# Optimization experiments

Measured on AMD Instinct MI355X. Metric: run time of the kernel, lower is better.

The kernel has to match this reference:

```python
import jax, jax.numpy as jnp
import numpy as np
import math

B, T, D, H = 4, 1024, 1024, 16
DK = D // H
TAU_THRESH = 0.3


def setup_inputs() -> dict:
    key = jax.random.key(0)
    ks = jax.random.split(key, 13)
    s = 1.0 / math.sqrt(D)
    return {
        "x": jax.random.normal(ks[0], (B, T, D), dtype=jnp.float32),
        "Wq": jax.random.normal(ks[1], (D, D), dtype=jnp.float32) * s,
        "bq": jax.random.normal(ks[2], (D,), dtype=jnp.float32) * s,
        "Wk": jax.random.normal(ks[3], (D, D), dtype=jnp.float32) * s,
        "bk": jax.random.normal(ks[4], (D,), dtype=jnp.float32) * s,
        "Wv": jax.random.normal(ks[5], (D, D), dtype=jnp.float32) * s,
        "bv": jax.random.normal(ks[6], (D,), dtype=jnp.float32) * s,
        "Wo": jax.random.normal(ks[7], (D, D), dtype=jnp.float32) * s,
        "bo": jax.random.normal(ks[8], (D,), dtype=jnp.float32) * s,
        "Wg1": jax.random.normal(ks[9], (1, D), dtype=jnp.float32) * s,
        "bg1": jax.random.normal(ks[10], (1,), dtype=jnp.float32) * s,
        "Wg2": jax.random.normal(ks[11], (1, D), dtype=jnp.float32) * s,
        "bg2": jax.random.normal(ks[12], (1,), dtype=jnp.float32) * s,
    }


def reference(x, Wq, bq, Wk, bk, Wv, bv, Wo, bo, Wg1, bg1, Wg2, bg2):
    b, t, d = x.shape
    # projections (torch Linear: y = x @ W.T + b)
    Q = (x @ Wq.T + bq).reshape(b, t, H, DK).transpose(0, 2, 1, 3)  # [B,H,T,dk]
    K = (x @ Wk.T + bk).reshape(b, t, H, DK).transpose(0, 2, 1, 3)
    V = (x @ Wv.T + bv).reshape(b, t, H, DK).transpose(0, 2, 1, 3)
    scores = jnp.einsum("bhqd,bhkd->bhqk", Q, K) / math.sqrt(DK)  # [B,H,T,T]
    # confidence gates from first-token query context [B, H*dk] = [B, D]
    context = Q[:, :, 0, :].reshape(b, d)
    q1 = jax.nn.sigmoid(context @ Wg1.T + bg1)  # [B,1]
    q2 = jax.nn.sigmoid(context @ Wg2.T + bg2)  # [B,1]
    c = jnp.clip(q1 * q2, 1e-8, 1.0)            # [B,1]
    tau = jnp.where(c < TAU_THRESH, 1.0 / c, jnp.ones_like(c)).reshape(b, 1, 1, 1)
    p = jax.nn.softmax(scores / tau, axis=-1)
    cb = c.reshape(b, 1, 1, 1)
    p_gated = cb * p + (1.0 - cb) * (1.0 / t)
    u = jnp.mean(1.0 - c, axis=-1, keepdims=True)  # [B,1]
    attn_out = jnp.einsum("bhqk,bhkd->bhqd", p_gated, V)
    attn_out = attn_out.transpose(0, 2, 1, 3).reshape(b, t, d)
    output = attn_out @ Wo.T + bo
    return output, u
```

## Files before the change

kernel.cpp:

```cpp
#include <hip/hip_runtime.h>
#include <stdint.h>

typedef short bf16x8 __attribute__((ext_vector_type(8)));
typedef float f32x4 __attribute__((ext_vector_type(4)));

#define MFMA_BF16(a, b, c) __builtin_amdgcn_mfma_f32_16x16x32_bf16((a), (b), (c), 0, 0, 0)

__device__ __forceinline__ short f2bf(float x) {
  union { float f; uint32_t u; } v; v.f = x;
  uint32_t r = (v.u + 0x7FFFu + ((v.u >> 16) & 1u)) >> 16;
  return (short)r;
}
__device__ __forceinline__ uint32_t rnd_bf_hi(float x) {
  union { float f; uint32_t u; } v; v.f = x;
  return v.u + 0x7FFFu + ((v.u >> 16) & 1u);
}
__device__ __forceinline__ uint32_t pack2bf(float a, float b) {
  return __builtin_amdgcn_perm(rnd_bf_hi(b), rnd_bf_hi(a), 0x07060302);
}
__device__ __forceinline__ float bfbits2f(uint32_t b16) {
  union { uint32_t u; float f; } v; v.u = b16 << 16; return v.f;
}
__device__ __forceinline__ float fexp2(float x) {
#if __has_builtin(__builtin_amdgcn_exp2f)
  return __builtin_amdgcn_exp2f(x);
#else
  return __expf(x * 0.6931471805599453f);
#endif
}
__device__ __forceinline__ void async16(const void* g, void* l) {
  __builtin_amdgcn_global_load_lds(
      (const __attribute__((address_space(1))) uint32_t*)g,
      (__attribute__((address_space(3))) uint32_t*)l, 16, 0, 0);
}

#define BAR() __builtin_amdgcn_s_barrier()
#define LGKM0() asm volatile("s_waitcnt lgkmcnt(0)" ::: "memory")
#define VMCNT(n) asm volatile("s_waitcnt vmcnt(" #n ")" ::: "memory")
#define PRIO1() __builtin_amdgcn_s_setprio(1)
#define PRIO0() __builtin_amdgcn_s_setprio(0)

__global__ __launch_bounds__(256) void prep_k(
    const float* __restrict__ x, const float* __restrict__ Wq,
    const float* __restrict__ Wk, const float* __restrict__ Wv,
    const float* __restrict__ Wo, const float* __restrict__ bq,
    short* __restrict__ xb, short* __restrict__ Wqb, short* __restrict__ Wkb,
    short* __restrict__ Wvb, short* __restrict__ Wob, float* __restrict__ ctx) {
  __shared__ float xs[1024];
  const int bid = blockIdx.x;
  const int tid = threadIdx.x;
  if (bid < 8192) {
    const float* src; short* dst; int idx;
    if (bid < 4096) {
      src = x; dst = xb; idx = (bid << 8) + tid;
    } else {
      const int r = bid - 4096;
      const int z = r >> 10;
      src = (z == 0) ? Wq : (z == 1) ? Wk : (z == 2) ? Wv : Wo;
      dst = (z == 0) ? Wqb : (z == 1) ? Wkb : (z == 2) ? Wvb : Wob;
      idx = ((r & 1023) << 8) + tid;
    }
    float4 v = ((const float4*)src)[idx];
    short4 o;
    o.x = f2bf(v.x); o.y = f2bf(v.y); o.z = f2bf(v.z); o.w = f2bf(v.w);
    ((short4*)dst)[idx] = o;
  } else {
    const int r = bid - 8192;
    const int b = r >> 4;
    const int n0 = (r & 15) << 6;
    for (int i = tid; i < 1024; i += 256) xs[i] = x[b * 1048576 + i];
    __syncthreads();
    const int w = tid >> 6, lane = tid & 63;
    const float4* xv4 = (const float4*)xs;
    for (int rr = 0; rr < 16; ++rr) {
      const int n = n0 + (w << 4) + rr;
      const float4* wrow = (const float4*)(Wq + n * 1024);
      float p = 0.f;
#pragma unroll
      for (int c2 = 0; c2 < 4; ++c2) {
        float4 wv = wrow[lane + (c2 << 6)];
        float4 xv = xv4[lane + (c2 << 6)];
        p += xv.x * wv.x + xv.y * wv.y + xv.z * wv.z + xv.w * wv.w;
      }
#pragma unroll
      for (int off = 32; off; off >>= 1) p += __shfl_xor(p, off);
      if (lane == 0) ctx[b * 1024 + n] = p + bq[n];
    }
  }
}

__global__ __launch_bounds__(256) void gates_fin(const float* __restrict__ ctx,
                                                 const float* __restrict__ Wg1,
                                                 const float* __restrict__ bg1,
                                                 const float* __restrict__ Wg2,
                                                 const float* __restrict__ bg2,
                                                 float* __restrict__ gates,
                                                 float* __restrict__ u_out) {
  __shared__ float red[16];
  const int tid = threadIdx.x, w = tid >> 6, lane = tid & 63;
  for (int b = 0; b < 4; ++b) {
    float4 cv = ((const float4*)(ctx + b * 1024))[tid];
    float4 w1 = ((const float4*)Wg1)[tid];
    float4 w2 = ((const float4*)Wg2)[tid];
    float p1 = cv.x * w1.x + cv.y * w1.y + cv.z * w1.z + cv.w * w1.w;
    float p2 = cv.x * w2.x + cv.y * w2.y + cv.z * w2.z + cv.w * w2.w;
#pragma unroll
    for (int off = 32; off; off >>= 1) { p1 += __shfl_xor(p1, off); p2 += __shfl_xor(p2, off); }
    if (lane == 0) { red[w] = p1; red[8 + w] = p2; }
    __syncthreads();
    if (tid == 0) {
      float g1 = red[0] + red[1] + red[2] + red[3] + bg1[0];
      float g2 = red[8] + red[9] + red[10] + red[11] + bg2[0];
      float q1 = 1.f / (1.f + expf(-g1));
      float q2 = 1.f / (1.f + expf(-g2));
      float c = fminf(fmaxf(q1 * q2, 1e-8f), 1.0f);
      gates[b * 2 + 0] = c;
      gates[b * 2 + 1] = (c < 0.3f ? c : 1.0f) * 0.125f * 1.4426950408889634f;
      u_out[b] = 1.0f - c;
    }
    __syncthreads();
  }
}

template <bool SWP>
__device__ __forceinline__ void qkv_core(const short* __restrict__ xb,
                                         const short* __restrict__ W,
                                         const float* __restrict__ bias,
                                         short* __restrict__ out,
                                         short* sm, int m0, int nl0) {
  const int tid = threadIdx.x;
  const int wid = tid >> 6, lane = tid & 63;
  const int wr = wid >> 2, wc = wid & 3;
  const int m15 = lane & 15, quad = lane >> 4;

  const int rowb = tid >> 3;
  const int c16 = (tid & 7) ^ (((tid >> 5) & 1) << 1);
  const short* aB = xb + (m0 + rowb) * 1024 + (c16 << 3);
  const short* bB = W + (nl0 + rowb) * 1024 + (c16 << 3);

  short* As = sm;
  short* Bs = sm + 32768;

#define STAGEH(sb, tt, hf, dst)                        \
  do {                                                 \
    const short* _s = (sb) + (hf)*131072 + (tt)*64;    \
    short* _d = (dst) + ((hf) << 13) + (tid << 3);     \
    async16(_s, _d);                                   \
    async16(_s + 65536, _d + 4096);                    \
  } while (0)

#define RD(base, f, kk)                                                        \
  (*(const bf16x8*)((base) + ((f) << 10) + (m15 << 6) +                        \
                    (((((kk) << 2) + quad) ^ ((m15 & 4) >> 1)) << 3)))

#define MM(accr, af, bf)                                   \
  do {                                                     \
    if (SWP) accr = MFMA_BF16((bf), (af), (accr));         \
    else     accr = MFMA_BF16((af), (bf), (accr));         \
  } while (0)

  f32x4 acc[8][4];
#pragma unroll
  for (int i = 0; i < 8; ++i)
#pragma unroll
    for (int j = 0; j < 4; ++j) { f32x4 zz = {0.f, 0.f, 0.f, 0.f}; acc[i][j] = zz; }

  STAGEH(bB, 0, 0, Bs);
  STAGEH(aB, 0, 0, As);
  STAGEH(aB, 0, 1, As);
  STAGEH(bB, 0, 1, Bs);
  STAGEH(bB, 1, 0, Bs + 16384);
  STAGEH(aB, 1, 0, As + 16384);
  VMCNT(4);
  BAR();

  bf16x8 a[4][2], b0[2][2], b1[2][2];

  for (int t = 0; t < 16; ++t) {
    const int buf = t & 1;
    const short* Ab = As + (buf << 14) + (wr << 13);
    const short* Bb = Bs + (buf << 14) + ((wc >> 1) << 13) + ((wc & 1) << 12);
    short* Adn = As + ((buf ^ 1) << 14);
    short* Bdn = Bs + ((buf ^ 1) << 14);
    short* Ad2 = As + (buf << 14);
    short* Bd2 = Bs + (buf << 14);

#pragma unroll
    for (int fi = 0; fi < 4; ++fi) { a[fi][0] = RD(Ab, fi, 0); a[fi][1] = RD(Ab, fi, 1); }
#pragma unroll
    for (int fj = 0; fj < 2; ++fj) { b0[fj][0] = RD(Bb, fj, 0); b0[fj][1] = RD(Bb, fj, 1); }
    if (t < 15) STAGEH(aB, t + 1, 1, Adn);
    BAR();
    LGKM0();
    PRIO1();
#pragma unroll
    for (int fi = 0; fi < 4; ++fi)
#pragma unroll
      for (int fj = 0; fj < 2; ++fj) {
        MM(acc[fi][fj], a[fi][0], b0[fj][0]);
        MM(acc[fi][fj], a[fi][1], b0[fj][1]);
      }
    PRIO0();
    BAR();

#pragma unroll
    for (int fj = 0; fj < 2; ++fj) { b1[fj][0] = RD(Bb, 2 + fj, 0); b1[fj][1] = RD(Bb, 2 + fj, 1); }
    if (t < 15) STAGEH(bB, t + 1, 1, Bdn);
    BAR();
    LGKM0();
    PRIO1();
#pragma unroll
    for (int fi = 0; fi < 4; ++fi)
#pragma unroll
      for (int fj = 0; fj < 2; ++fj) {
        MM(acc[fi][2 + fj], a[fi][0], b1[fj][0]);
        MM(acc[fi][2 + fj], a[fi][1], b1[fj][1]);
      }
    PRIO0();
    BAR();

#pragma unroll
    for (int fi = 0; fi < 4; ++fi) { a[fi][0] = RD(Ab, 4 + fi, 0); a[fi][1] = RD(Ab, 4 + fi, 1); }
    if (t < 14) STAGEH(bB, t + 2, 0, Bd2);
    BAR();
    LGKM0();
    PRIO1();
#pragma unroll
    for (int fi = 0; fi < 4; ++fi)
#pragma unroll
      for (int fj = 0; fj < 2; ++fj) {
        MM(acc[4 + fi][2 + fj], a[fi][0], b1[fj][0]);
        MM(acc[4 + fi][2 + fj], a[fi][1], b1[fj][1]);
      }
    PRIO0();
    BAR();

    if (t < 14) STAGEH(aB, t + 2, 0, Ad2);
    BAR();
    PRIO1();
#pragma unroll
    for (int fi = 0; fi < 4; ++fi)
#pragma unroll
      for (int fj = 0; fj < 2; ++fj) {
        MM(acc[4 + fi][fj], a[fi][0], b0[fj][0]);
        MM(acc[4 + fi][fj], a[fi][1], b0[fj][1]);
      }
    PRIO0();
    if (t < 14) { VMCNT(4); }
    else if (t == 14) { VMCNT(0); }
    BAR();
  }

  const int nw = nl0 + (wc << 6);
  if (SWP) {
#pragma unroll
    for (int fj = 0; fj < 4; ++fj) {
      const int n = nw + (fj << 4) + (quad << 2);
      const float4 bv = *(const float4*)(bias + n);
      const int hh = n >> 6, dk0 = n & 63;
#pragma unroll
      for (int fi = 0; fi < 8; ++fi) {
        const int m = m0 + (wr << 7) + (fi << 4) + m15;
        const int bb = m >> 10, tt = m & 1023;
        uint2 st;
        st.x = pack2bf(acc[fi][fj][0] + bv.x, acc[fi][fj][1] + bv.y);
        st.y = pack2bf(acc[fi][fj][2] + bv.z, acc[fi][fj][3] + bv.w);
        *(uint2*)(out + (((bb << 4) + hh) << 16) + (tt << 6) + dk0) = st;
      }
    }
  } else {
#pragma unroll
    for (int fj = 0; fj < 4; ++fj) {
      const int n = nw + (fj << 4) + m15;
      const float bv = bias[n];
      const int hh = n >> 6, dk = n & 63;
#pragma unroll
      for (int fi = 0; fi < 8; ++fi) {
        const int m = m0 + (wr << 7) + (fi << 4) + (quad << 2);
        const int bb = m >> 10, t0 = m & 1023;
        uint2 st;
        st.x = pack2bf(acc[fi][fj][0] + bv, acc[fi][fj][1] + bv);
        st.y = pack2bf(acc[fi][fj][2] + bv, acc[fi][fj][3] + bv);
        *(uint2*)(out + (((bb << 4) + hh) << 16) + (dk << 10) + t0) = st;
      }
    }
  }
#undef STAGEH
#undef RD
#undef MM
}

__global__ __launch_bounds__(512) void gemm_qkv8(
    const short* __restrict__ xb,
    const short* __restrict__ Wqb, const short* __restrict__ Wkb, const short* __restrict__ Wvb,
    const float* __restrict__ bq, const float* __restrict__ bk, const float* __restrict__ bv,
    short* __restrict__ Qh, short* __restrict__ Kh, short* __restrict__ Vt) {
  const int lin = blockIdx.x;
  const int s = ((lin & 7) * 24) + (lin >> 3);
  const int bx = s & 15, by = s >> 4;
  const int z = by >> 2;
  const int m0 = bx << 8, nl0 = (by & 3) << 8;
  extern __shared__ short sm[];
  if (z == 0)      qkv_core<true >(xb, Wqb, bq, Qh, sm, m0, nl0);
  else if (z == 1) qkv_core<true >(xb, Wkb, bk, Kh, sm, m0, nl0);
  else             qkv_core<false>(xb, Wvb, bv, Vt, sm, m0, nl0);
}

__global__ __launch_bounds__(256) void gemm_out(const short* __restrict__ Ab,
                                                const short* __restrict__ Wo,
                                                const float* __restrict__ bo,
                                                float* __restrict__ Cout) {
  const int m0 = blockIdx.x << 7;
  const int n0 = blockIdx.y << 7;
  const int tid = threadIdx.x;
  const int w = tid >> 6, lane = tid & 63;
  const int m15 = lane & 15, quad = lane >> 4;
  const int wr = w >> 1, wc = w & 1;

  __shared__ short As[4096];
  __shared__ short Bs[4096];

  f32x4 acc[4][4];
#pragma unroll
  for (int i = 0; i < 4; ++i)
#pragma unroll
    for (int j = 0; j < 4; ++j) { f32x4 zz = {0.f, 0.f, 0.f, 0.f}; acc[i][j] = zz; }

  const int srow = (w << 5) + (lane >> 2);
  const int scol = (lane & 3) << 3;
  const short* ga0 = Ab + (m0 + srow) * 1024 + scol;
  const short* ga1 = ga0 + 16 * 1024;
  const short* gb0 = Wo + (n0 + srow) * 1024 + scol;
  const short* gb1 = gb0 + 16 * 1024;
  short* la0 = &As[srow * 32 + scol];
  short* la1 = la0 + 512;
  short* lb0 = &Bs[srow * 32 + scol];
  short* lb1 = lb0 + 512;

  for (int kt = 0; kt < 32; ++kt) {
    async16(ga0, la0); async16(ga1, la1);
    async16(gb0, lb0); async16(gb1, lb1);
    ga0 += 32; ga1 += 32; gb0 += 32; gb1 += 32;
    __syncthreads();
    bf16x8 a[4], b[4];
#pragma unroll
    for (int i = 0; i < 4; ++i)
      a[i] = *(const bf16x8*)(&As[((wr << 6) + (i << 4) + m15) * 32 + (quad << 3)]);
#pragma unroll
    for (int j = 0; j < 4; ++j)
      b[j] = *(const bf16x8*)(&Bs[((wc << 6) + (j << 4) + m15) * 32 + (quad << 3)]);
#pragma unroll
    for (int i = 0; i < 4; ++i)
#pragma unroll
      for (int j = 0; j < 4; ++j)
        acc[i][j] = MFMA_BF16(a[i], b[j], acc[i][j]);
    __syncthreads();
  }

#pragma unroll
  for (int j = 0; j < 4; ++j) {
    const int n = n0 + (wc << 6) + (j << 4) + m15;
    const float bb_ = bo[n];
#pragma unroll
    for (int i = 0; i < 4; ++i) {
      const int mb = m0 + (wr << 6) + (i << 4) + (quad << 2);
#pragma unroll
      for (int r = 0; r < 4; ++r)
        Cout[(mb + r) * 1024 + n] = acc[i][j][r] + bb_;
    }
  }
}

__global__ __launch_bounds__(256, 2) void attn_k(const short* __restrict__ Qh,
                                                 const short* __restrict__ Kh,
                                                 const short* __restrict__ Vt,
                                                 const float* __restrict__ gates,
                                                 short* __restrict__ attnb) {
  const int bh = blockIdx.x;
  const int b = bh >> 4, h = bh & 15;
  const int q0 = blockIdx.y << 7;
  const int tid = threadIdx.x;
  const int w = tid >> 6, lane = tid & 63;
  const int m15 = lane & 15, quad = lane >> 4;

  __shared__ short Ks[2][4096];
  __shared__ short Vs[2][4096];

  const short* ksrc = Kh + bh * 65536;
  const short* vsrc = Vt + bh * 65536;

  const float sl = gates[b * 2 + 1];

  const short* qsrcA = Qh + ((bh << 10) + q0 + (w << 4) + m15) * 64;
  const short* qsrcB = qsrcA + 64 * 64;
  const bf16x8 qA0 = *(const bf16x8*)(qsrcA + (quad << 3));
  const bf16x8 qA1 = *(const bf16x8*)(qsrcA + 32 + (quad << 3));
  const bf16x8 qB0 = *(const bf16x8*)(qsrcB + (quad << 3));
  const bf16x8 qB1 = *(const bf16x8*)(qsrcB + 32 + (quad << 3));

  const bf16x8 vone = {0x3F80, 0x3F80, 0x3F80, 0x3F80, 0x3F80, 0x3F80, 0x3F80, 0x3F80};

  const int off0 = tid, off1 = tid + 256;
  const int r0 = off0 >> 3, cb0 = (off0 & 7) ^ (r0 & 7);
  const int r1 = off1 >> 3, cb1 = (off1 & 7) ^ (r1 & 7);

#define STAGE(kv, bufi)                                                        \
  do {                                                                         \
    async16(ksrc + (((kv) << 6) + r0) * 64 + (cb0 << 3), &Ks[bufi][off0 << 3]);\
    async16(ksrc + (((kv) << 6) + r1) * 64 + (cb1 << 3), &Ks[bufi][off1 << 3]);\
    async16(vsrc + r0 * 1024 + ((kv) << 6) + (cb0 << 3), &Vs[bufi][off0 << 3]);\
    async16(vsrc + r1 * 1024 + ((kv) << 6) + (cb1 << 3), &Vs[bufi][off1 << 3]);\
  } while (0)

  STAGE(0, 0);

  float lsumA = 0.f, lsumB = 0.f;
  f32x4 oA[4], oB[4], o_mv[4];
#pragma unroll
  for (int jd = 0; jd < 4; ++jd) {
    f32x4 zz = {0.f, 0.f, 0.f, 0.f};
    oA[jd] = zz; oB[jd] = zz; o_mv[jd] = zz;
  }

  const int srcA = ((quad & 1) << 5) + m15;
  const int srcB = srcA + 16;
  const bool selhi = (quad & 2) != 0;

#define BUILD_PF(pf, pk)                                                       \
  do {                                                                         \
    _Pragma("unroll")                                                          \
    for (int Hh = 0; Hh < 2; ++Hh) {                                           \
      uint32_t f[4];                                                           \
      _Pragma("unroll")                                                        \
      for (int rp = 0; rp < 2; ++rp) {                                         \
        uint32_t alo = (uint32_t)__shfl((int)pk[2 * Hh][rp], srcA);            \
        uint32_t ahi = (uint32_t)__shfl((int)pk[2 * Hh + 1][rp], srcA);        \
        uint32_t blo = (uint32_t)__shfl((int)pk[2 * Hh][rp], srcB);            \
        uint32_t bhi = (uint32_t)__shfl((int)pk[2 * Hh + 1][rp], srcB);        \
        f[rp]     = selhi ? ahi : alo;                                         \
        f[2 + rp] = selhi ? bhi : blo;                                         \
      }                                                                        \
      pf[Hh] = *(bf16x8*)f;                                                    \
    }                                                                          \
  } while (0)

  for (int kv = 0; kv < 16; ++kv) {
    __syncthreads();
    if (kv < 15) STAGE(kv + 1, (kv + 1) & 1);
    const short* Kb = &Ks[kv & 1][0];
    const short* Vb = &Vs[kv & 1][0];

    f32x4 sA[4], sB[4];
#pragma unroll
    for (int s = 0; s < 4; ++s) {
      const int row = (s << 4) + m15;
      const int sw = row & 7;
      bf16x8 a0 = *(const bf16x8*)(Kb + (row << 6) + ((quad ^ sw) << 3));
      bf16x8 a1 = *(const bf16x8*)(Kb + (row << 6) + (((quad + 4) ^ sw) << 3));
      f32x4 zA = {0.f, 0.f, 0.f, 0.f};
      zA = MFMA_BF16(a0, qA0, zA);
      zA = MFMA_BF16(a1, qA1, zA);
      sA[s] = zA;
      f32x4 zB = {0.f, 0.f, 0.f, 0.f};
      zB = MFMA_BF16(a0, qB0, zB);
      zB = MFMA_BF16(a1, qB1, zB);
      sB[s] = zB;
    }

    uint32_t pkA[4][2], pkB[4][2];
#pragma unroll
    for (int s = 0; s < 4; ++s) {
      float a0 = fexp2(sA[s][0] * sl);
      float a1 = fexp2(sA[s][1] * sl);
      float a2 = fexp2(sA[s][2] * sl);
      float a3 = fexp2(sA[s][3] * sl);
      lsumA += (a0 + a1) + (a2 + a3);
      pkA[s][0] = pack2bf(a0, a1);
      pkA[s][1] = pack2bf(a2, a3);
      float b0 = fexp2(sB[s][0] * sl);
      float b1 = fexp2(sB[s][1] * sl);
      float b2 = fexp2(sB[s][2] * sl);
      float b3 = fexp2(sB[s][3] * sl);
      lsumB += (b0 + b1) + (b2 + b3);
      pkB[s][0] = pack2bf(b0, b1);
      pkB[s][1] = pack2bf(b2, b3);
    }

    bf16x8 pfA[2], pfB[2];
    BUILD_PF(pfA, pkA);
    BUILD_PF(pfB, pkB);

#pragma unroll
    for (int jd = 0; jd < 4; ++jd) {
      const int row = (jd << 4) + m15;
      const int sw = row & 7;
      bf16x8 v0 = *(const bf16x8*)(Vb + (row << 6) + ((quad ^ sw) << 3));
      bf16x8 v1 = *(const bf16x8*)(Vb + (row << 6) + (((quad + 4) ^ sw) << 3));
      oA[jd] = MFMA_BF16(v0, pfA[0], oA[jd]);
      oA[jd] = MFMA_BF16(v1, pfA[1], oA[jd]);
      oB[jd] = MFMA_BF16(v0, pfB[0], oB[jd]);
      oB[jd] = MFMA_BF16(v1, pfB[1], oB[jd]);
      o_mv[jd] = MFMA_BF16(v0, vone, o_mv[jd]);
      o_mv[jd] = MFMA_BF16(v1, vone, o_mv[jd]);
    }
  }
#undef STAGE
#undef BUILD_PF

  float lA = lsumA;
  lA += __shfl_xor(lA, 16);
  lA += __shfl_xor(lA, 32);
  float lB = lsumB;
  lB += __shfl_xor(lB, 16);
  lB += __shfl_xor(lB, 32);

  const float cg = gates[b * 2 + 0];
  const float sc0A = cg / lA;
  const float sc0B = cg / lB;
  const float coef = (1.0f - cg) * (1.0f / 1024.0f);
  const int qrowA = q0 + (w << 4) + m15;
  short* orowA = attnb + ((b << 10) + qrowA) * 1024 + (h << 6);
  short* orowB = orowA + 64 * 1024;
#pragma unroll
  for (int jd = 0; jd < 4; ++jd) {
    uint2 stA;
    stA.x = pack2bf(sc0A * oA[jd][0] + coef * o_mv[jd][0],
                    sc0A * oA[jd][1] + coef * o_mv[jd][1]);
    stA.y = pack2bf(sc0A * oA[jd][2] + coef * o_mv[jd][2],
                    sc0A * oA[jd][3] + coef * o_mv[jd][3]);
    *(uint2*)(orowA + (jd << 4) + (quad << 2)) = stA;
    uint2 stB;
    stB.x = pack2bf(sc0B * oB[jd][0] + coef * o_mv[jd][0],
                    sc0B * oB[jd][1] + coef * o_mv[jd][1]);
    stB.y = pack2bf(sc0B * oB[jd][2] + coef * o_mv[jd][2],
                    sc0B * oB[jd][3] + coef * o_mv[jd][3]);
    *(uint2*)(orowB + (jd << 4) + (quad << 2)) = stB;
  }
}

extern "C" void kernel_launch(void* const* d_in, const int* in_sizes, int n_in,
                              void* d_out, int out_size, void* d_ws, size_t ws_size,
                              hipStream_t stream) {
  const float* x   = (const float*)d_in[0];
  const float* Wq  = (const float*)d_in[1];
  const float* bq  = (const float*)d_in[2];
  const float* Wk  = (const float*)d_in[3];
  const float* bk  = (const float*)d_in[4];
  const float* Wv  = (const float*)d_in[5];
  const float* bv  = (const float*)d_in[6];
  const float* Wo  = (const float*)d_in[7];
  const float* bo  = (const float*)d_in[8];
  const float* Wg1 = (const float*)d_in[9];
  const float* bg1 = (const float*)d_in[10];
  const float* Wg2 = (const float*)d_in[11];
  const float* bg2 = (const float*)d_in[12];
  float* out = (float*)d_out;

  char* ws = (char*)d_ws;
  short* xb   = (short*)(ws + 0);
  short* Wqb  = (short*)(ws + 8388608);
  short* Wkb  = (short*)(ws + 10485760);
  short* Wvb  = (short*)(ws + 12582912);
  short* Wob  = (short*)(ws + 14680064);
  short* Qh   = (short*)(ws + 16777216);
  short* Kh   = (short*)(ws + 25165824);
  short* Vt   = (short*)(ws + 33554432);
  short* attb = (short*)(ws + 41943040);
  float* ctx  = (float*)(ws + 50331648);
  float* gat  = (float*)(ws + 50348032);

  static bool lds_inited = false;
  if (!lds_inited) {
    hipFuncSetAttribute(reinterpret_cast<const void*>(gemm_qkv8),
                        hipFuncAttributeMaxDynamicSharedMemorySize, 131072);
    lds_inited = true;
  }

  prep_k<<<8256, 256, 0, stream>>>(x, Wq, Wk, Wv, Wo, bq,
                                   xb, Wqb, Wkb, Wvb, Wob, ctx);
  gates_fin<<<1, 256, 0, stream>>>(ctx, Wg1, bg1, Wg2, bg2, gat, out + 4194304);

  gemm_qkv8<<<192, 512, 131072, stream>>>(xb, Wqb, Wkb, Wvb, bq, bk, bv,
                                          Qh, Kh, Vt);
  attn_k<<<dim3(64, 8), 256, 0, stream>>>(Qh, Kh, Vt, gat, attb);
  gemm_out<<<dim3(32, 8), 256, 0, stream>>>(attb, Wob, bo, out);
}
```

Baseline: 213.8 us.

## Software-pipeline PV MFMA behind next QK and widen LDS swizzle in QKV GEMM

The attention loop now defers the P·V MFMAs by one iteration, issuing the previous tile's PV products right after the current QK^T MFMAs. The intent is to overlap the exp/pack/shuffle work with matrix-core activity. V gets a triple-buffered LDS ring so the deferred tile is not overwritten by the next prefetch. Separately, the QKV GEMM staging switches to a full 3-bit XOR swizzle on row index to cut LDS bank conflicts. The cost is more LDS, extra live registers for the carried P fragments, and a possible occupancy drop.

```diff
diff --git a/kernel.cpp b/kernel.cpp
--- a/kernel.cpp
+++ b/kernel.cpp
@@ -132,11 +132,12 @@
   const int wid = tid >> 6, lane = tid & 63;
   const int wr = wid >> 2, wc = wid & 3;
   const int m15 = lane & 15, quad = lane >> 4;
+  const int swz = m15 & 7;
 
   const int rowb = tid >> 3;
-  const int c16 = (tid & 7) ^ (((tid >> 5) & 1) << 1);
-  const short* aB = xb + (m0 + rowb) * 1024 + (c16 << 3);
-  const short* bB = W + (nl0 + rowb) * 1024 + (c16 << 3);
+  const int cs = ((tid & 7) ^ (rowb & 7)) << 3;
+  const short* aB = xb + (m0 + rowb) * 1024 + cs;
+  const short* bB = W + (nl0 + rowb) * 1024 + cs;
 
   short* As = sm;
   short* Bs = sm + 32768;
@@ -151,7 +152,7 @@
 
 #define RD(base, f, kk)                                                        \
   (*(const bf16x8*)((base) + ((f) << 10) + (m15 << 6) +                        \
-                    (((((kk) << 2) + quad) ^ ((m15 & 4) >> 1)) << 3)))
+                    (((((kk) << 2) + quad) ^ swz) << 3)))
 
 #define MM(accr, af, bf)                                   \
   do {                                                     \
@@ -384,7 +385,7 @@
   const int m15 = lane & 15, quad = lane >> 4;
 
   __shared__ short Ks[2][4096];
-  __shared__ short Vs[2][4096];
+  __shared__ short Vs[3][4096];
 
   const short* ksrc = Kh + bh * 65536;
   const short* vsrc = Vt + bh * 65536;
@@ -404,15 +405,15 @@
   const int r0 = off0 >> 3, cb0 = (off0 & 7) ^ (r0 & 7);
   const int r1 = off1 >> 3, cb1 = (off1 & 7) ^ (r1 & 7);
 
-#define STAGE(kv, bufi)                                                        \
+#define STAGE(kv, kb, vb)                                                      \
   do {                                                                         \
-    async16(ksrc + (((kv) << 6) + r0) * 64 + (cb0 << 3), &Ks[bufi][off0 << 3]);\
-    async16(ksrc + (((kv) << 6) + r1) * 64 + (cb1 << 3), &Ks[bufi][off1 << 3]);\
-    async16(vsrc + r0 * 1024 + ((kv) << 6) + (cb0 << 3), &Vs[bufi][off0 << 3]);\
-    async16(vsrc + r1 * 1024 + ((kv) << 6) + (cb1 << 3), &Vs[bufi][off1 << 3]);\
+    async16(ksrc + (((kv) << 6) + r0) * 64 + (cb0 << 3), &Ks[kb][off0 << 3]);  \
+    async16(ksrc + (((kv) << 6) + r1) * 64 + (cb1 << 3), &Ks[kb][off1 << 3]);  \
+    async16(vsrc + r0 * 1024 + ((kv) << 6) + (cb0 << 3), &Vs[vb][off0 << 3]);  \
+    async16(vsrc + r1 * 1024 + ((kv) << 6) + (cb1 << 3), &Vs[vb][off1 << 3]);  \
   } while (0)
 
-  STAGE(0, 0);
+  STAGE(0, 0, 0);
 
   float lsumA = 0.f, lsumB = 0.f;
   f32x4 oA[4], oB[4], o_mv[4];
@@ -444,11 +445,31 @@
     }                                                                          \
   } while (0)
 
+#define PV_STEP(Vb, pfa, pfb)                                                  \
+  do {                                                                         \
+    _Pragma("unroll")                                                          \
+    for (int jd = 0; jd < 4; ++jd) {                                           \
+      const int row = (jd << 4) + m15;                                         \
+      const int sw = row & 7;                                                  \
+      bf16x8 v0 = *(const bf16x8*)((Vb) + (row << 6) + ((quad ^ sw) << 3));    \
+      bf16x8 v1 = *(const bf16x8*)((Vb) + (row << 6) + (((quad + 4) ^ sw) << 3)); \
+      oA[jd] = MFMA_BF16(v0, pfa[0], oA[jd]);                                  \
+      oA[jd] = MFMA_BF16(v1, pfa[1], oA[jd]);                                  \
+      oB[jd] = MFMA_BF16(v0, pfb[0], oB[jd]);                                  \
+      oB[jd] = MFMA_BF16(v1, pfb[1], oB[jd]);                                  \
+      o_mv[jd] = MFMA_BF16(v0, vone, o_mv[jd]);                                \
+      o_mv[jd] = MFMA_BF16(v1, vone, o_mv[jd]);                                \
+    }                                                                          \
+  } while (0)
+
+  bf16x8 pfpA[2], pfpB[2];
+  pfpA[0] = (bf16x8){0,0,0,0,0,0,0,0}; pfpA[1] = pfpA[0];
+  pfpB[0] = pfpA[0]; pfpB[1] = pfpA[0];
+
   for (int kv = 0; kv < 16; ++kv) {
     __syncthreads();
-    if (kv < 15) STAGE(kv + 1, (kv + 1) & 1);
+    if (kv < 15) STAGE(kv + 1, (kv + 1) & 1, (kv + 1) % 3);
     const short* Kb = &Ks[kv & 1][0];
-    const short* Vb = &Vs[kv & 1][0];
 
     f32x4 sA[4], sB[4];
 #pragma unroll
@@ -465,6 +486,11 @@
       zB = MFMA_BF16(a0, qB0, zB);
       zB = MFMA_BF16(a1, qB1, zB);
       sB[s] = zB;
+    }
+
+    if (kv > 0) {
+      const short* Vb = &Vs[(kv - 1) % 3][0];
+      PV_STEP(Vb, pfpA, pfpB);
     }
 
     uint32_t pkA[4][2], pkB[4][2];
@@ -489,23 +515,17 @@
     bf16x8 pfA[2], pfB[2];
     BUILD_PF(pfA, pkA);
     BUILD_PF(pfB, pkB);
-
-#pragma unroll
-    for (int jd = 0; jd < 4; ++jd) {
-      const int row = (jd << 4) + m15;
-      const int sw = row & 7;
-      bf16x8 v0 = *(const bf16x8*)(Vb + (row << 6) + ((quad ^ sw) << 3));
-      bf16x8 v1 = *(const bf16x8*)(Vb + (row << 6) + (((quad + 4) ^ sw) << 3));
-      oA[jd] = MFMA_BF16(v0, pfA[0], oA[jd]);
-      oA[jd] = MFMA_BF16(v1, pfA[1], oA[jd]);
-      oB[jd] = MFMA_BF16(v0, pfB[0], oB[jd]);
-      oB[jd] = MFMA_BF16(v1, pfB[1], oB[jd]);
-      o_mv[jd] = MFMA_BF16(v0, vone, o_mv[jd]);
-      o_mv[jd] = MFMA_BF16(v1, vone, o_mv[jd]);
-    }
+    pfpA[0] = pfA[0]; pfpA[1] = pfA[1];
+    pfpB[0] = pfB[0]; pfpB[1] = pfB[1];
+  }
+
+  {
+    const short* Vb = &Vs[15 % 3][0];
+    PV_STEP(Vb, pfpA, pfpB);
   }
 #undef STAGE
 #undef BUILD_PF
+#undef PV_STEP
 
   float lA = lsumA;
   lA += __shfl_xor(lA, 16);
```

New measurement: 209.6 us. 1.02x faster.
